# Kernel tuning notes

Measured on AMD Instinct MI355X. Metric: run time of the kernel, lower is better.

The kernel has to match this reference:

```python
import jax, jax.numpy as jnp
import numpy as np

N = 100000   # nodes
E = 1600000  # edges
D = 128      # input_dim
H = 128      # hidden_dim
CH = 16      # cluster_hidden_dim
P = 10       # processor_nodes


def setup_inputs() -> dict:
    key = jax.random.key(0)
    ks = jax.random.split(key, 22)
    s = 0.05
    return {
        "x": jax.random.normal(ks[0], (N, D), jnp.float32),
        "edges": jax.random.randint(ks[1], (2, E), 0, N, dtype=jnp.int32),
        "edge_attr": jax.random.uniform(ks[2], (E,), jnp.float32),
        "ready": jax.random.randint(ks[3], (N, 1), 0, 2, dtype=jnp.int32),
        "proc_emb": jax.random.normal(ks[4], (P, 3), jnp.float32),
        # GCN layers (PyG GCNConv: lin without bias, explicit bias added after aggregation)
        "gcn_w": jax.random.normal(ks[5], (2, D, H), jnp.float32) * s,
        "gcn_b": jax.random.normal(ks[6], (2, H), jnp.float32) * s,
        # listmlp: Linear(H,H) -> relu, then Linear(H,1)
        "mlp_w1": jax.random.normal(ks[7], (H, H), jnp.float32) * s,
        "mlp_b1": jax.random.normal(ks[8], (H,), jnp.float32) * s,
        "mlp_w2": jax.random.normal(ks[9], (H, 1), jnp.float32) * s,
        "mlp_b2": jax.random.normal(ks[10], (1,), jnp.float32) * s,
        # listmlp_value: Linear(H,1)
        "val_w": jax.random.normal(ks[11], (H, 1), jnp.float32) * s,
        "val_b": jax.random.normal(ks[12], (1,), jnp.float32) * s,
        # cluster_linear: Linear(3*P, CH)
        "cl_w": jax.random.normal(ks[13], (3 * P, CH), jnp.float32) * s,
        "cl_b": jax.random.normal(ks[14], (CH,), jnp.float32) * s,
        # listmlp_pass: Linear(H+CH,H) -> relu, then Linear(H,1)
        "pass_w1": jax.random.normal(ks[15], (H + CH, H), jnp.float32) * s,
        "pass_b1": jax.random.normal(ks[16], (H,), jnp.float32) * s,
        "pass_w2": jax.random.normal(ks[17], (H, 1), jnp.float32) * s,
        "pass_b2": jax.random.normal(ks[18], (1,), jnp.float32) * s,
    }


def _gcn_layer(x, row, col, w_e, W, b):
    # PyG GCNConv with flow='target_to_source': out[row] += norm_e * (x @ W)[col]
    # gcn_norm with idx=row: deg[i] = sum of edge weights with row==i (self-loops included)
    h = x @ W                                              # [N,H]
    deg = jax.ops.segment_sum(w_e, row, num_segments=N)    # [N]
    dis = jnp.where(deg > 0, jax.lax.rsqrt(deg), 0.0)      # deg^-1/2, inf -> 0
    norm = dis[row] * w_e * dis[col]                       # [E+N]
    msg = h[col] * norm[:, None]                           # [E+N,H] gather
    out = jax.ops.segment_sum(msg, row, num_segments=N)    # [N,H] scatter-add
    return out + b


def _forward(x, edges, edge_attr, ready, proc_emb, gcn_w, gcn_b,
             mlp_w1, mlp_b1, mlp_w2, mlp_b2, val_w, val_b, cl_w, cl_b,
             pass_w1, pass_b1, pass_w2, pass_b2):
    # add self-loops with weight 1 (GCNConv default add_self_loops=True)
    loop = jnp.arange(N, dtype=edges.dtype)
    row = jnp.concatenate([edges[0], loop])
    col = jnp.concatenate([edges[1], loop])
    w_e = jnp.concatenate([edge_attr, jnp.ones((N,), edge_attr.dtype)])

    h = x
    for l in range(2):
        h = jax.nn.relu(_gcn_layer(h, row, col, w_e, gcn_w[l], gcn_b[l]))

    mask = ready[:, 0] > 0                                 # [N] bool
    v = jnp.mean(h, axis=0)                                # [H]
    x_pass = jnp.max(jnp.where(mask[:, None], h, -jnp.inf), axis=0)  # masked max, [H]

    fc = proc_emb.reshape(-1) @ cl_w + cl_b                # [CH]
    x_pass = jnp.concatenate([x_pass, fc], axis=0)         # [H+CH]

    v = v @ val_w + val_b                                  # [1]

    logits = jax.nn.relu(h @ mlp_w1 + mlp_b1) @ mlp_w2 + mlp_b2        # [N,1]
    x_pass = jax.nn.relu(x_pass @ pass_w1 + pass_b1) @ pass_w2 + pass_b2  # [1]

    # torch indexes logits[ready]; here we mask non-ready entries with -inf so
    # the softmax over [N+1] matches torch's values on the ready rows.
    node_logits = jnp.where(mask, logits[:, 0], -jnp.inf)
    probs = jax.nn.softmax(jnp.concatenate([node_logits, x_pass], axis=0))  # [N+1]
    return probs, v


def reference(x, edges, edge_attr, ready, proc_emb, gcn_w, gcn_b,
              mlp_w1, mlp_b1, mlp_w2, mlp_b2, val_w, val_b, cl_w, cl_b,
              pass_w1, pass_b1, pass_w2, pass_b2):
    return _forward(x, edges, edge_attr, ready, proc_emb, gcn_w, gcn_b,
                    mlp_w1, mlp_b1, mlp_w2, mlp_b2, val_w, val_b, cl_w, cl_b,
                    pass_w1, pass_b1, pass_w2, pass_b2)
```

## Files before the change

kernel.cpp:

```cpp
#include <hip/hip_runtime.h>
#include <cstdint>

#define NN 100000
#define EE 1600000
#define HH 128
#define NREP 8
#define PSZ (NN / 8)
#define SS 64
#define CAP 300000
#define NBB 500
#define BCH 3200
#define SCAN_CHUNK 512
#define NSCAN ((NN + SCAN_CHUNK - 1) / SCAN_CHUNK)

typedef unsigned long long u64;
typedef unsigned short ushort;
typedef unsigned char uchar;
typedef __attribute__((ext_vector_type(8))) short bf16x8;
typedef __attribute__((ext_vector_type(4))) float f32x4;
typedef __attribute__((ext_vector_type(2))) float f32x2;

__device__ __forceinline__ ushort f2bf(float x) {
    union { float f; unsigned u; } v; v.f = x;
    unsigned r = v.u + 0x7fffu + ((v.u >> 16) & 1u);
    return (ushort)(r >> 16);
}
__device__ __forceinline__ float bf2f(unsigned h16) {
    union { unsigned u; float f; } v; v.u = h16 << 16; return v.f;
}

__device__ __forceinline__ uchar f2fp8(float a) {
    return (uchar)(__builtin_amdgcn_cvt_pk_fp8_f32(a, a, 0, false) & 0xff);
}
__device__ __forceinline__ void unpack8_fp8(uint2 q, float* v) {
    f32x2 a = __builtin_amdgcn_cvt_pk_f32_fp8(q.x, false);
    f32x2 b = __builtin_amdgcn_cvt_pk_f32_fp8(q.x, true);
    f32x2 c = __builtin_amdgcn_cvt_pk_f32_fp8(q.y, false);
    f32x2 d = __builtin_amdgcn_cvt_pk_f32_fp8(q.y, true);
    v[0] = a[0]; v[1] = a[1]; v[2] = b[0]; v[3] = b[1];
    v[4] = c[0]; v[5] = c[1]; v[6] = d[0]; v[7] = d[1];
}

__device__ __forceinline__ unsigned encf(float f) {
    int b = __float_as_int(f);
    return (b >= 0) ? ((unsigned)b | 0x80000000u) : ~(unsigned)b;
}
__device__ __forceinline__ float decf(unsigned u) {
    return (u & 0x80000000u) ? __int_as_float((int)(u & 0x7fffffffu))
                             : __int_as_float((int)(~u));
}
#define ENC_NEG_INF 0x007FFFFFu

__global__ void k_init(float* __restrict__ meansum, unsigned* __restrict__ maxenc,
                       unsigned* __restrict__ lmaxenc, float* __restrict__ esum,
                       int* __restrict__ gtail) {
    int i = blockIdx.x * blockDim.x + threadIdx.x;
    if (i < NREP * HH) { meansum[i] = 0.f; maxenc[i] = ENC_NEG_INF; }
    if (i < 8) gtail[i] = 0;
    if (i == 0) { lmaxenc[0] = ENC_NEG_INF; esum[0] = 0.f; }
}

__global__ void k_prep(const float* __restrict__ w0, const float* __restrict__ w1,
                       const float* __restrict__ w2, ushort* __restrict__ wt) {
    int idx = blockIdx.x * blockDim.x + threadIdx.x;
    if (idx >= 3 * HH * HH) return;
    int mat = idx >> 14;
    int e = idx & 16383;
    int n = e >> 7, k = e & 127;
    const float* src = (mat == 0) ? w0 : (mat == 1) ? w1 : w2;
    wt[idx] = f2bf(src[k * HH + n]);
}

__global__ __launch_bounds__(256) void k_bucket(const int* __restrict__ rows,
                                                const int* __restrict__ cols,
                                                const float* __restrict__ ea,
                                                int* __restrict__ gtail,
                                                u64* __restrict__ ebuck) {
    __shared__ u64 buf[8][1024];
    __shared__ int cnt8[8];
    __shared__ int rsv[8];
    int t = threadIdx.x;
    if (t < 8) cnt8[t] = 0;
    __syncthreads();
    int e0 = blockIdx.x * BCH;
    int e1 = e0 + BCH;
    for (int ebase = e0; ebase < e1; ebase += 1024) {
        int e = ebase + t * 4;
        if (e < e1) {
            int4 r4 = *(const int4*)(rows + e);
            int4 c4 = *(const int4*)(cols + e);
            float4 a4 = *(const float4*)(ea + e);
            int rr[4] = {r4.x, r4.y, r4.z, r4.w};
            int cc[4] = {c4.x, c4.y, c4.z, c4.w};
            float aa[4] = {a4.x, a4.y, a4.z, a4.w};
#pragma unroll
            for (int j = 0; j < 4; ++j) {
                int p = rr[j] / PSZ;
                int rl = rr[j] - p * PSZ;
                unsigned q = (unsigned)(aa[j] * 32767.0f + 0.5f);
                u64 en = ((u64)rl << 32) | (u64)(((unsigned)cc[j] << 15) | q);
                int idx = atomicAdd(&cnt8[p], 1);
                buf[p][idx] = en;
            }
        }
        __syncthreads();
        if (t < 8) rsv[t] = atomicAdd(&gtail[t], cnt8[t]);
        __syncthreads();
#pragma unroll
        for (int p = 0; p < 8; ++p) {
            int nn = cnt8[p], oo = rsv[p];
            u64* dst = ebuck + (size_t)p * CAP + oo;
            for (int j = t; j < nn; j += 256) dst[j] = buf[p][j];
        }
        __syncthreads();
        if (t < 8) cnt8[t] = 0;
        __syncthreads();
    }
}

__global__ __launch_bounds__(256) void k_cnt2(const u64* __restrict__ ebuck,
                                              const int* __restrict__ gtail,
                                              int* __restrict__ cnt) {
    __shared__ unsigned h32[PSZ / 2];
    int b = blockIdx.x;
    int s = b >> 3, p = b & 7;
    for (int j = threadIdx.x; j < PSZ / 2; j += 256) h32[j] = 0;
    __syncthreads();
    int pc = gtail[p];
    int len = (pc + SS - 1) / SS;
    int lo = s * len, hi = min(lo + len, pc);
    const u64* src = ebuck + (size_t)p * CAP;
    for (int i = lo + threadIdx.x; i < hi; i += 256) {
        int rl = (int)(src[i] >> 32);
        atomicAdd(&h32[rl >> 1], (rl & 1) ? 0x10000u : 1u);
    }
    __syncthreads();
    int* dst = cnt + (size_t)(p * SS + s) * PSZ;
    for (int j = threadIdx.x; j < PSZ / 2; j += 256) {
        unsigned v = h32[j];
        ((int2*)dst)[j] = make_int2((int)(v & 0xffffu), (int)(v >> 16));
    }
}

__global__ void k_rowsum(const int* __restrict__ cnt, int* __restrict__ count) {
    int r = blockIdx.x * blockDim.x + threadIdx.x;
    if (r >= NN) return;
    int p = r / PSZ, rl = r - p * PSZ;
    int s = 0;
#pragma unroll 8
    for (int c = 0; c < SS; ++c) s += cnt[(size_t)(p * SS + c) * PSZ + rl];
    count[r] = s;
}

__global__ void k_scan1(const int* __restrict__ cnt, int* __restrict__ out,
                        int* __restrict__ bsum) {
    int b = blockIdx.x, t = threadIdx.x;
    int i0 = b * SCAN_CHUNK + t * 2;
    int c0 = (i0 < NN) ? cnt[i0] : 0;
    int c1 = (i0 + 1 < NN) ? cnt[i0 + 1] : 0;
    int s = c0 + c1;
    int lane = t & 63, w = t >> 6;
    int v = s;
#pragma unroll
    for (int off = 1; off < 64; off <<= 1) {
        int u = __shfl_up(v, off, 64);
        if (lane >= off) v += u;
    }
    __shared__ int wsum[4];
    if (lane == 63) wsum[w] = v;
    __syncthreads();
    int wadd = 0;
    for (int j = 0; j < w; ++j) wadd += wsum[j];
    int incl = v + wadd;
    int excl = incl - s;
    if (i0 < NN) out[i0] = excl;
    if (i0 + 1 < NN) out[i0 + 1] = excl + c0;
    if (t == 255) bsum[b] = incl;
}

__global__ void k_scan2(int* __restrict__ bsum) {
    __shared__ int tmp[256];
    int t = threadIdx.x;
    int v = (t < NSCAN) ? bsum[t] : 0;
    tmp[t] = v;
    __syncthreads();
    for (int off = 1; off < 256; off <<= 1) {
        int u = (t >= off) ? tmp[t - off] : 0;
        __syncthreads();
        tmp[t] += u;
        __syncthreads();
    }
    if (t < NSCAN) bsum[t] = tmp[t] - v;
}

__global__ void k_scan3(int* __restrict__ out, const int* __restrict__ bsum) {
    int i = blockIdx.x * blockDim.x + threadIdx.x;
    if (i < NN) out[i] += bsum[i / SCAN_CHUNK];
    if (i == 0) out[NN] = EE;
}

__global__ void k_makeptr(const int* __restrict__ cnt, const int* __restrict__ base,
                          int* __restrict__ fillptr) {
    int r = blockIdx.x * blockDim.x + threadIdx.x;
    if (r >= NN) return;
    int p = r / PSZ, rl = r - p * PSZ;
    int acc = base[r];
#pragma unroll 8
    for (int c = 0; c < SS; ++c) {
        fillptr[(size_t)(p * SS + c) * PSZ + rl] = acc;
        acc += cnt[(size_t)(p * SS + c) * PSZ + rl];
    }
}

__global__ __launch_bounds__(256) void k_fill2(const u64* __restrict__ ebuck,
                                               const int* __restrict__ gtail,
                                               const int* __restrict__ fillptr,
                                               unsigned* __restrict__ csre) {
    __shared__ int nxt[PSZ];
    int b = blockIdx.x;
    int s = b >> 3, p = b & 7;
    const int* fsrc = fillptr + (size_t)(p * SS + s) * PSZ;
    for (int j = threadIdx.x; j < PSZ; j += 256) nxt[j] = fsrc[j];
    __syncthreads();
    int pc = gtail[p];
    int len = (pc + SS - 1) / SS;
    int lo = s * len, hi = min(lo + len, pc);
    const u64* src = ebuck + (size_t)p * CAP;
    for (int i = lo + threadIdx.x; i < hi; i += 256) {
        u64 en = src[i];
        int rl = (int)(en >> 32);
        int slot = atomicAdd(&nxt[rl], 1);
        csre[slot] = (unsigned)(en & 0xffffffffu);
    }
}

__global__ void k_degsum(const unsigned* __restrict__ csre, const int* __restrict__ base,
                         float* __restrict__ dis) {
    int r = blockIdx.x * blockDim.x + threadIdx.x;
    if (r >= NN) return;
    int lo = base[r], hi = base[r + 1];
    float s = 0.f;
    for (int e = lo; e < hi; ++e) s += (float)(csre[e] & 0x7fffu);
    dis[r] = rsqrtf(1.0f + s * (1.0f / 32767.0f));
}

__global__ __launch_bounds__(256) void k_gather(const uchar* __restrict__ hW,
                                                const unsigned* __restrict__ csre,
                                                const int* __restrict__ base,
                                                const float* __restrict__ dis,
                                                const float* __restrict__ bias,
                                                ushort* __restrict__ agg) {
    int node = blockIdx.x * 16 + (threadIdx.x >> 4);
    if (node >= NN) return;
    int l = threadIdx.x & 15;
    int f = l * 8;
    int lo = base[node], hi = base[node + 1];
    float disn = dis[node];
    float wk = disn * (1.0f / 32767.0f);
    const unsigned SELF = (unsigned)node << 15;
    float acc[8];
    {
        uint2 q = *(const uint2*)(hW + (size_t)node * HH + f);
        float v[8]; unpack8_fp8(q, v);
#pragma unroll
        for (int j = 0; j < 8; ++j) acc[j] = disn * v[j];
    }
    for (int eb = lo; eb < hi; eb += 4) {
        unsigned pp[4];
#pragma unroll
        for (int j = 0; j < 4; ++j) {
            int e = eb + j;
            pp[j] = (e < hi) ? csre[e] : SELF;
        }
        uint2 qq[4];
#pragma unroll
        for (int j = 0; j < 4; ++j)
            qq[j] = *(const uint2*)(hW + (size_t)(pp[j] >> 15) * HH + f);
#pragma unroll
        for (int j = 0; j < 4; ++j) {
            float w = (float)(pp[j] & 0x7fffu) * wk;
            float v[8]; unpack8_fp8(qq[j], v);
#pragma unroll
            for (int k = 0; k < 8; ++k) acc[k] += w * v[k];
        }
    }
    float4 b0 = *(const float4*)(bias + f);
    float4 b1 = *(const float4*)(bias + f + 4);
    ushort o[8];
    o[0] = f2bf(acc[0] + b0.x); o[1] = f2bf(acc[1] + b0.y);
    o[2] = f2bf(acc[2] + b0.z); o[3] = f2bf(acc[3] + b0.w);
    o[4] = f2bf(acc[4] + b1.x); o[5] = f2bf(acc[5] + b1.y);
    o[6] = f2bf(acc[6] + b1.z); o[7] = f2bf(acc[7] + b1.w);
    *(uint4*)(agg + (size_t)node * HH + f) = *(uint4*)o;
}

template <int MODE>
__global__ __launch_bounds__(256) void k_mfma(const void* __restrict__ Ain,
                                              const ushort* __restrict__ Wt,
                                              uchar* __restrict__ C,
                                              const float* __restrict__ dis,
                                              const float* __restrict__ b1,
                                              const float* __restrict__ w2v,
                                              const float* __restrict__ b2,
                                              const int* __restrict__ ready,
                                              float* __restrict__ logits,
                                              float* __restrict__ meansum,
                                              unsigned* __restrict__ maxenc,
                                              unsigned* __restrict__ lmaxenc, int n) {
    __shared__ ushort As[64 * HH];
    __shared__ ushort Ws[128 * HH];
    __shared__ int rdy[64];
    __shared__ unsigned slmax;
    const int t = threadIdx.x;
    const int rb = blockIdx.x * 64;
    if (MODE == 2) {
        if (t < 64) rdy[t] = (rb + t < n) ? ready[rb + t] : 0;
        if (t == 0) slmax = ENC_NEG_INF;
    }
#pragma unroll
    for (int i = 0; i < 8; ++i) {
        int nr = i * 16 + (t >> 4);
        int gc = t & 15;
        uint4 q = *(const uint4*)(Wt + (size_t)nr * HH + gc * 8);
        *(uint4*)(Ws + nr * HH + ((gc ^ (nr & 15)) * 8)) = q;
    }
#pragma unroll
    for (int i = 0; i < 4; ++i) {
        int m = i * 16 + (t >> 4);
        int k = (t & 15) * 8;
        ushort pk[8];
        if (MODE == 0) {
            const float* Af = (const float*)Ain;
            float4 v0 = make_float4(0.f, 0.f, 0.f, 0.f), v1 = v0;
            if (rb + m < n) {
                const float* src = Af + (size_t)(rb + m) * HH + k;
                v0 = *(const float4*)src;
                v1 = *(const float4*)(src + 4);
            }
            pk[0] = f2bf(v0.x); pk[1] = f2bf(v0.y); pk[2] = f2bf(v0.z); pk[3] = f2bf(v0.w);
            pk[4] = f2bf(v1.x); pk[5] = f2bf(v1.y); pk[6] = f2bf(v1.z); pk[7] = f2bf(v1.w);
        } else {
            const ushort* Au = (const ushort*)Ain;
            uint4 q = make_uint4(0, 0, 0, 0);
            if (rb + m < n) q = *(const uint4*)(Au + (size_t)(rb + m) * HH + k);
            *(uint4*)pk = q;
#pragma unroll
            for (int j = 0; j < 8; ++j) pk[j] = (pk[j] & 0x8000) ? (ushort)0 : pk[j];
        }
        int gsw = (t & 15) ^ (m & 15);
        *(uint4*)(As + m * HH + gsw * 8) = *(uint4*)pk;
    }
    __syncthreads();

    const int wave = t >> 6, lane = t & 63;
    const int cl = lane & 15;
    const int kq = lane >> 4;
    const int m0 = wave * 16;

    f32x4 acc[8];
#pragma unroll
    for (int c = 0; c < 8; ++c) acc[c] = (f32x4){0.f, 0.f, 0.f, 0.f};

    const int am = m0 + cl;
#pragma unroll
    for (int kk = 0; kk < 4; ++kk) {
        int g = kk * 4 + kq;
        bf16x8 a = *(const bf16x8*)(As + am * HH + ((g ^ cl) * 8));
#pragma unroll
        for (int c = 0; c < 8; ++c) {
            bf16x8 b = *(const bf16x8*)(Ws + (c * 16 + cl) * HH + ((g ^ cl) * 8));
            acc[c] = __builtin_amdgcn_mfma_f32_16x16x32_bf16(a, b, acc[c], 0, 0, 0);
        }
    }

    if (MODE < 2) {
#pragma unroll
        for (int r = 0; r < 4; ++r) {
            int row = rb + m0 + kq * 4 + r;
            if (row < n) {
                float dsc = dis[row];
#pragma unroll
                for (int c = 0; c < 8; ++c)
                    C[(size_t)row * HH + c * 16 + cl] = f2fp8(acc[c][r] * dsc);
            }
        }
    } else {
        float b1c[8], w2c[8];
#pragma unroll
        for (int c = 0; c < 8; ++c) { b1c[c] = b1[c * 16 + cl]; w2c[c] = w2v[c * 16 + cl]; }
        const float b2s = b2[0];
        unsigned mylmax = ENC_NEG_INF;
#pragma unroll
        for (int r = 0; r < 4; ++r) {
            float s = 0.f;
#pragma unroll
            for (int c = 0; c < 8; ++c)
                s += fmaxf(acc[c][r] + b1c[c], 0.f) * w2c[c];
            s += __shfl_xor(s, 1, 64);
            s += __shfl_xor(s, 2, 64);
            s += __shfl_xor(s, 4, 64);
            s += __shfl_xor(s, 8, 64);
            if (cl == 0) {
                int rloc = m0 + kq * 4 + r;
                int row = rb + rloc;
                if (row < n) {
                    float lg = s + b2s;
                    logits[row] = lg;
                    if (rdy[rloc] > 0) {
                        unsigned e = encf(lg);
                        if (e > mylmax) mylmax = e;
                    }
                }
            }
        }
        if (cl == 0 && mylmax != ENC_NEG_INF) atomicMax(&slmax, mylmax);

        int lim = min(64, n - rb);
        if (t < HH) {
            int f = t, gf = f >> 3, fo = f & 7;
            float sum = 0.f, mx = -3.4e38f;
            for (int m = 0; m < lim; ++m) {
                float v = bf2f(As[m * HH + ((gf ^ (m & 15)) * 8) + fo]);
                sum += v;
                if (rdy[m] > 0) mx = fmaxf(mx, v);
            }
            int rep = blockIdx.x & (NREP - 1);
            atomicAdd(&meansum[rep * HH + f], sum);
            if (mx > -3.0e38f) atomicMax(&maxenc[rep * HH + f], encf(mx));
        }
        __syncthreads();
        if (t == 0 && slmax != ENC_NEG_INF) atomicMax(lmaxenc, slmax);
    }
}

__global__ void k_fin1(const float* __restrict__ meansum, const unsigned* __restrict__ maxenc,
                       const unsigned* __restrict__ lmaxenc,
                       const float* __restrict__ val_w, const float* __restrict__ val_b,
                       const float* __restrict__ pe, const float* __restrict__ cl_w,
                       const float* __restrict__ cl_b, const float* __restrict__ pw1,
                       const float* __restrict__ pb1, const float* __restrict__ pw2,
                       const float* __restrict__ pb2, float* __restrict__ scal,
                       float* __restrict__ d_out) {
    __shared__ float xp[144];
    __shared__ float msum[HH];
    __shared__ float zp[HH];
    int t = threadIdx.x;
    if (t < HH) {
        float s = 0.f;
        unsigned mx = ENC_NEG_INF;
#pragma unroll
        for (int r = 0; r < NREP; ++r) {
            s += meansum[r * HH + t];
            unsigned e = maxenc[r * HH + t];
            if (e > mx) mx = e;
        }
        msum[t] = s;
        xp[t] = decf(mx);
    } else if (t < 144) {
        int c = t - HH;
        float s = cl_b[c];
        for (int k = 0; k < 30; ++k) s += pe[k] * cl_w[k * 16 + c];
        xp[t] = s;
    }
    __syncthreads();
    if (t < HH) {
        float s = pb1[t];
        for (int k = 0; k < 144; ++k) s += xp[k] * pw1[k * HH + t];
        zp[t] = fmaxf(s, 0.f);
    }
    __syncthreads();
    if (t < 64) {
        float s1 = zp[t] * pw2[t] + zp[t + 64] * pw2[t + 64];
        float s2 = msum[t] * val_w[t] + msum[t + 64] * val_w[t + 64];
#pragma unroll
        for (int off = 32; off > 0; off >>= 1) {
            s1 += __shfl_xor(s1, off, 64);
            s2 += __shfl_xor(s2, off, 64);
        }
        if (t == 0) {
            float xpass = s1 + pb2[0];
            float v = s2 * (1.0f / NN) + val_b[0];
            float M = fmaxf(decf(lmaxenc[0]), xpass);
            scal[0] = M;
            scal[1] = expf(xpass - M);
            d_out[NN + 1] = v;
        }
    }
}

__global__ __launch_bounds__(256) void k_exp(const float* __restrict__ logits,
                                             const int* __restrict__ ready,
                                             const float* __restrict__ scal,
                                             float* __restrict__ d_out,
                                             float* __restrict__ esum) {
    __shared__ float warr[4];
    int t = threadIdx.x;
    int i = blockIdx.x * 256 + t;
    float M = scal[0];
    float p = 0.f;
    if (i < NN) {
        if (ready[i] > 0) p = expf(logits[i] - M);
        d_out[i] = p;
    }
    float s = p;
#pragma unroll
    for (int off = 32; off > 0; off >>= 1) s += __shfl_xor(s, off, 64);
    if ((t & 63) == 0) warr[t >> 6] = s;
    __syncthreads();
    if (t == 0) atomicAdd(esum, warr[0] + warr[1] + warr[2] + warr[3]);
}

__global__ void k_scale(const float* __restrict__ esum, const float* __restrict__ scal,
                        float* __restrict__ d_out) {
    int i = blockIdx.x * blockDim.x + threadIdx.x;
    float inv = 1.0f / (esum[0] + scal[1]);
    if (i < NN) d_out[i] *= inv;
    else if (i == NN) d_out[NN] = scal[1] * inv;
}

extern "C" void kernel_launch(void* const* d_in, const int* in_sizes, int n_in,
                              void* d_out, int out_size, void* d_ws, size_t ws_size,
                              hipStream_t stream) {
    const float* x      = (const float*)d_in[0];
    const int*   edges  = (const int*)d_in[1];
    const float* eattr  = (const float*)d_in[2];
    const int*   ready  = (const int*)d_in[3];
    const float* pe     = (const float*)d_in[4];
    const float* gcn_w  = (const float*)d_in[5];
    const float* gcn_b  = (const float*)d_in[6];
    const float* mlp_w1 = (const float*)d_in[7];
    const float* mlp_b1 = (const float*)d_in[8];
    const float* mlp_w2 = (const float*)d_in[9];
    const float* mlp_b2 = (const float*)d_in[10];
    const float* val_w  = (const float*)d_in[11];
    const float* val_b  = (const float*)d_in[12];
    const float* cl_w   = (const float*)d_in[13];
    const float* cl_b   = (const float*)d_in[14];
    const float* pw1    = (const float*)d_in[15];
    const float* pb1    = (const float*)d_in[16];
    const float* pw2    = (const float*)d_in[17];
    const float* pb2    = (const float*)d_in[18];

    const int* rows = edges;
    const int* cols = edges + EE;

    char* P = (char*)d_ws;
    size_t off = 0;
    auto carve = [&](size_t bytes) {
        off = (off + 255) & ~(size_t)255;
        void* p = P + off;
        off += bytes;
        return p;
    };
    float* dis     = (float*)carve(NN * 4);
    float* logits  = (float*)carve(NN * 4);
    int*   count   = (int*)carve(NN * 4);
    int*   base    = (int*)carve((NN + 1) * 4);
    int*   bsum    = (int*)carve(256 * 4);
    ushort* bufB   = (ushort*)carve((size_t)NN * HH * 2);
    uchar* bufH    = (uchar*)carve((size_t)NN * HH);
    unsigned* csre = (unsigned*)carve((size_t)EE * 4);
    u64*   ebuck   = (u64*)carve((size_t)8 * CAP * 8);
    int*   fillptr = (int*)carve((size_t)8 * SS * PSZ * 4);
    float* meansum = (float*)carve(NREP * HH * 4);
    unsigned* maxenc = (unsigned*)carve(NREP * HH * 4);
    unsigned* lmaxenc = (unsigned*)carve(4);
    float* esum    = (float*)carve(4);
    float* scal    = (float*)carve(8);
    int*   gtail   = (int*)carve(8 * 4);
    ushort* wt     = (ushort*)carve(3 * HH * HH * 2);

    int* cnt = (int*)bufB;

    float* out = (float*)d_out;

    const int nb = (NN + 255) / 256;
    const int gb = (NN + 63) / 64;
    const int ab = (NN + 15) / 16;
    const int pb = 8 * SS;

    k_init<<<(NREP * HH + 255) / 256, 256, 0, stream>>>(meansum, maxenc, lmaxenc, esum, gtail);
    k_prep<<<(3 * HH * HH + 255) / 256, 256, 0, stream>>>(gcn_w, gcn_w + HH * HH, mlp_w1, wt);

    k_bucket<<<NBB, 256, 0, stream>>>(rows, cols, eattr, gtail, ebuck);
    k_cnt2<<<pb, 256, 0, stream>>>(ebuck, gtail, cnt);
    k_rowsum<<<nb, 256, 0, stream>>>(cnt, count);
    k_scan1<<<NSCAN, 256, 0, stream>>>(count, base, bsum);
    k_scan2<<<1, 256, 0, stream>>>(bsum);
    k_scan3<<<nb, 256, 0, stream>>>(base, bsum);
    k_makeptr<<<nb, 256, 0, stream>>>(cnt, base, fillptr);
    k_fill2<<<pb, 256, 0, stream>>>(ebuck, gtail, fillptr, csre);
    k_degsum<<<nb, 256, 0, stream>>>(csre, base, dis);

    k_mfma<0><<<gb, 256, 0, stream>>>(x, wt, bufH, dis, nullptr, nullptr, nullptr, nullptr,
                                      nullptr, nullptr, nullptr, nullptr, NN);
    k_gather<<<ab, 256, 0, stream>>>(bufH, csre, base, dis, gcn_b, bufB);

    k_mfma<1><<<gb, 256, 0, stream>>>(bufB, wt + HH * HH, bufH, dis, nullptr, nullptr, nullptr,
                                      nullptr, nullptr, nullptr, nullptr, nullptr, NN);
    k_gather<<<ab, 256, 0, stream>>>(bufH, csre, base, dis, gcn_b + HH, bufB);

    k_mfma<2><<<gb, 256, 0, stream>>>(bufB, wt + 2 * HH * HH, nullptr, nullptr, mlp_b1, mlp_w2,
                                      mlp_b2, ready, logits, meansum, maxenc, lmaxenc, NN);
    k_fin1<<<1, 256, 0, stream>>>(meansum, maxenc, lmaxenc, val_w, val_b, pe, cl_w, cl_b,
                                  pw1, pb1, pw2, pb2, scal, out);
    k_exp<<<nb, 256, 0, stream>>>(logits, ready, scal, out, esum);
    k_scale<<<(NN + 1 + 255) / 256, 256, 0, stream>>>(esum, scal, out);
}
```

Measured before the change: 361.5 us.

## Pack per-slice row counts as 16-bit pairs and fold fill pointers into prefix deltas

The per-slice histograms are now stored as packed 16-bit pairs instead of expanded ints. A single row-delta kernel computes both row totals and per-slice exclusive prefix deltas, so k_makeptr and the large fillptr array are removed; k_fill2 rebuilds pointers from base plus delta. It also merges the init and weight-prep kernels into one launch, and unrolls the gather edge loop to 8 with clamped loads and zero weights for the tail. This cuts memory traffic and launch count in CSR construction, with a 16-bit count limit per slice that is assumed to hold.

```diff
diff --git a/kernel.cpp b/kernel.cpp
--- a/kernel.cpp
+++ b/kernel.cpp
@@ -6,6 +6,7 @@
 #define HH 128
 #define NREP 8
 #define PSZ (NN / 8)
+#define HPP (PSZ / 2)
 #define SS 64
 #define CAP 300000
 #define NBB 500
@@ -51,24 +52,22 @@
 }
 #define ENC_NEG_INF 0x007FFFFFu
 
-__global__ void k_init(float* __restrict__ meansum, unsigned* __restrict__ maxenc,
-                       unsigned* __restrict__ lmaxenc, float* __restrict__ esum,
-                       int* __restrict__ gtail) {
-    int i = blockIdx.x * blockDim.x + threadIdx.x;
-    if (i < NREP * HH) { meansum[i] = 0.f; maxenc[i] = ENC_NEG_INF; }
-    if (i < 8) gtail[i] = 0;
-    if (i == 0) { lmaxenc[0] = ENC_NEG_INF; esum[0] = 0.f; }
-}
-
-__global__ void k_prep(const float* __restrict__ w0, const float* __restrict__ w1,
-                       const float* __restrict__ w2, ushort* __restrict__ wt) {
+__global__ void k_setup(float* __restrict__ meansum, unsigned* __restrict__ maxenc,
+                        unsigned* __restrict__ lmaxenc, float* __restrict__ esum,
+                        int* __restrict__ gtail,
+                        const float* __restrict__ w0, const float* __restrict__ w1,
+                        const float* __restrict__ w2, ushort* __restrict__ wt) {
     int idx = blockIdx.x * blockDim.x + threadIdx.x;
-    if (idx >= 3 * HH * HH) return;
-    int mat = idx >> 14;
-    int e = idx & 16383;
-    int n = e >> 7, k = e & 127;
-    const float* src = (mat == 0) ? w0 : (mat == 1) ? w1 : w2;
-    wt[idx] = f2bf(src[k * HH + n]);
+    if (idx < NREP * HH) { meansum[idx] = 0.f; maxenc[idx] = ENC_NEG_INF; }
+    if (idx < 8) gtail[idx] = 0;
+    if (idx == 0) { lmaxenc[0] = ENC_NEG_INF; esum[0] = 0.f; }
+    if (idx < 3 * HH * HH) {
+        int mat = idx >> 14;
+        int e = idx & 16383;
+        int n = e >> 7, k = e & 127;
+        const float* src = (mat == 0) ? w0 : (mat == 1) ? w1 : w2;
+        wt[idx] = f2bf(src[k * HH + n]);
+    }
 }
 
 __global__ __launch_bounds__(256) void k_bucket(const int* __restrict__ rows,
@@ -120,11 +119,11 @@
 
 __global__ __launch_bounds__(256) void k_cnt2(const u64* __restrict__ ebuck,
                                               const int* __restrict__ gtail,
-                                              int* __restrict__ cnt) {
-    __shared__ unsigned h32[PSZ / 2];
+                                              unsigned* __restrict__ cntp) {
+    __shared__ unsigned h32[HPP];
     int b = blockIdx.x;
     int s = b >> 3, p = b & 7;
-    for (int j = threadIdx.x; j < PSZ / 2; j += 256) h32[j] = 0;
+    for (int j = threadIdx.x; j < HPP; j += 256) h32[j] = 0;
     __syncthreads();
     int pc = gtail[p];
     int len = (pc + SS - 1) / SS;
@@ -135,21 +134,26 @@
         atomicAdd(&h32[rl >> 1], (rl & 1) ? 0x10000u : 1u);
     }
     __syncthreads();
-    int* dst = cnt + (size_t)(p * SS + s) * PSZ;
-    for (int j = threadIdx.x; j < PSZ / 2; j += 256) {
-        unsigned v = h32[j];
-        ((int2*)dst)[j] = make_int2((int)(v & 0xffffu), (int)(v >> 16));
-    }
-}
-
-__global__ void k_rowsum(const int* __restrict__ cnt, int* __restrict__ count) {
-    int r = blockIdx.x * blockDim.x + threadIdx.x;
-    if (r >= NN) return;
-    int p = r / PSZ, rl = r - p * PSZ;
-    int s = 0;
+    unsigned* dst = cntp + (size_t)(p * SS + s) * HPP;
+    for (int j = threadIdx.x; j < HPP; j += 256) dst[j] = h32[j];
+}
+
+__global__ void k_rowdelta(const unsigned* __restrict__ cntp, int* __restrict__ count,
+                           unsigned* __restrict__ deltap) {
+    int rp = blockIdx.x * blockDim.x + threadIdx.x;
+    if (rp >= NN / 2) return;
+    int p = rp / HPP, j = rp - p * HPP;
+    unsigned s0 = 0, s1 = 0;
 #pragma unroll 8
-    for (int c = 0; c < SS; ++c) s += cnt[(size_t)(p * SS + c) * PSZ + rl];
-    count[r] = s;
+    for (int c = 0; c < SS; ++c) {
+        size_t o = (size_t)(p * SS + c) * HPP + j;
+        unsigned v = cntp[o];
+        deltap[o] = s0 | (s1 << 16);
+        s0 += v & 0xffffu;
+        s1 += v >> 16;
+    }
+    int r0 = p * PSZ + 2 * j;
+    *(int2*)(count + r0) = make_int2((int)s0, (int)s1);
 }
 
 __global__ void k_scan1(const int* __restrict__ cnt, int* __restrict__ out,
@@ -199,28 +203,22 @@
     if (i == 0) out[NN] = EE;
 }
 
-__global__ void k_makeptr(const int* __restrict__ cnt, const int* __restrict__ base,
-                          int* __restrict__ fillptr) {
-    int r = blockIdx.x * blockDim.x + threadIdx.x;
-    if (r >= NN) return;
-    int p = r / PSZ, rl = r - p * PSZ;
-    int acc = base[r];
-#pragma unroll 8
-    for (int c = 0; c < SS; ++c) {
-        fillptr[(size_t)(p * SS + c) * PSZ + rl] = acc;
-        acc += cnt[(size_t)(p * SS + c) * PSZ + rl];
-    }
-}
-
 __global__ __launch_bounds__(256) void k_fill2(const u64* __restrict__ ebuck,
                                                const int* __restrict__ gtail,
-                                               const int* __restrict__ fillptr,
+                                               const unsigned* __restrict__ deltap,
+                                               const int* __restrict__ base,
                                                unsigned* __restrict__ csre) {
     __shared__ int nxt[PSZ];
     int b = blockIdx.x;
     int s = b >> 3, p = b & 7;
-    const int* fsrc = fillptr + (size_t)(p * SS + s) * PSZ;
-    for (int j = threadIdx.x; j < PSZ; j += 256) nxt[j] = fsrc[j];
+    const unsigned* dsrc = deltap + (size_t)(p * SS + s) * HPP;
+    const int* bsrc = base + p * PSZ;
+    for (int j = threadIdx.x; j < HPP; j += 256) {
+        unsigned d = dsrc[j];
+        int2 bb = *(const int2*)(bsrc + 2 * j);
+        nxt[2 * j] = bb.x + (int)(d & 0xffffu);
+        nxt[2 * j + 1] = bb.y + (int)(d >> 16);
+    }
     __syncthreads();
     int pc = gtail[p];
     int len = (pc + SS - 1) / SS;
@@ -257,7 +255,6 @@
     int lo = base[node], hi = base[node + 1];
     float disn = dis[node];
     float wk = disn * (1.0f / 32767.0f);
-    const unsigned SELF = (unsigned)node << 15;
     float acc[8];
     {
         uint2 q = *(const uint2*)(hW + (size_t)node * HH + f);
@@ -265,20 +262,18 @@
 #pragma unroll
         for (int j = 0; j < 8; ++j) acc[j] = disn * v[j];
     }
-    for (int eb = lo; eb < hi; eb += 4) {
-        unsigned pp[4];
-#pragma unroll
-        for (int j = 0; j < 4; ++j) {
-            int e = eb + j;
-            pp[j] = (e < hi) ? csre[e] : SELF;
-        }
-        uint2 qq[4];
-#pragma unroll
-        for (int j = 0; j < 4; ++j)
+    for (int eb = lo; eb < hi; eb += 8) {
+        unsigned pp[8];
+#pragma unroll
+        for (int j = 0; j < 8; ++j)
+            pp[j] = csre[min(eb + j, hi - 1)];
+        uint2 qq[8];
+#pragma unroll
+        for (int j = 0; j < 8; ++j)
             qq[j] = *(const uint2*)(hW + (size_t)(pp[j] >> 15) * HH + f);
 #pragma unroll
-        for (int j = 0; j < 4; ++j) {
-            float w = (float)(pp[j] & 0x7fffu) * wk;
+        for (int j = 0; j < 8; ++j) {
+            float w = (eb + j < hi) ? (float)(pp[j] & 0x7fffu) * wk : 0.f;
             float v[8]; unpack8_fp8(qq[j], v);
 #pragma unroll
             for (int k = 0; k < 8; ++k) acc[k] += w * v[k];
@@ -561,7 +556,6 @@
     uchar* bufH    = (uchar*)carve((size_t)NN * HH);
     unsigned* csre = (unsigned*)carve((size_t)EE * 4);
     u64*   ebuck   = (u64*)carve((size_t)8 * CAP * 8);
-    int*   fillptr = (int*)carve((size_t)8 * SS * PSZ * 4);
     float* meansum = (float*)carve(NREP * HH * 4);
     unsigned* maxenc = (unsigned*)carve(NREP * HH * 4);
     unsigned* lmaxenc = (unsigned*)carve(4);
@@ -570,7 +564,8 @@
     int*   gtail   = (int*)carve(8 * 4);
     ushort* wt     = (ushort*)carve(3 * HH * HH * 2);
 
-    int* cnt = (int*)bufB;
+    unsigned* cntp   = (unsigned*)bufB;
+    unsigned* deltap = (unsigned*)bufB + (size_t)8 * SS * HPP;
 
     float* out = (float*)d_out;
 
@@ -579,17 +574,17 @@
     const int ab = (NN + 15) / 16;
     const int pb = 8 * SS;
 
-    k_init<<<(NREP * HH + 255) / 256, 256, 0, stream>>>(meansum, maxenc, lmaxenc, esum, gtail);
-    k_prep<<<(3 * HH * HH + 255) / 256, 256, 0, stream>>>(gcn_w, gcn_w + HH * HH, mlp_w1, wt);
+    k_setup<<<(3 * HH * HH + 255) / 256, 256, 0, stream>>>(meansum, maxenc, lmaxenc, esum,
+                                                           gtail, gcn_w, gcn_w + HH * HH,
+                                                           mlp_w1, wt);
 
     k_bucket<<<NBB, 256, 0, stream>>>(rows, cols, eattr, gtail, ebuck);
-    k_cnt2<<<pb, 256, 0, stream>>>(ebuck, gtail, cnt);
-    k_rowsum<<<nb, 256, 0, stream>>>(cnt, count);
+    k_cnt2<<<pb, 256, 0, stream>>>(ebuck, gtail, cntp);
+    k_rowdelta<<<(NN / 2 + 255) / 256, 256, 0, stream>>>(cntp, count, deltap);
     k_scan1<<<NSCAN, 256, 0, stream>>>(count, base, bsum);
     k_scan2<<<1, 256, 0, stream>>>(bsum);
     k_scan3<<<nb, 256, 0, stream>>>(base, bsum);
-    k_makeptr<<<nb, 256, 0, stream>>>(cnt, base, fillptr);
-    k_fill2<<<pb, 256, 0, stream>>>(ebuck, gtail, fillptr, csre);
+    k_fill2<<<pb, 256, 0, stream>>>(ebuck, gtail, deltap, base, csre);
     k_degsum<<<nb, 256, 0, stream>>>(csre, base, dis);
 
     k_mfma<0><<<gb, 256, 0, stream>>>(x, wt, bufH, dis, nullptr, nullptr, nullptr, nullptr,
```

Measured after the change: 337.6 us. -6.6%, faster.
